# Performance work log

Measured on AMD Instinct MI355X. Metric: run time of the kernel, lower is better.

The kernel has to match this reference:

```python
import jax, jax.numpy as jnp
import numpy as np

BINS = 10
LOSS_WEIGHT = 1.0


def setup_inputs() -> dict:
    key = jax.random.key(0)
    k1, k2 = jax.random.split(key)
    N, C = 32768, 1024
    pred = jax.random.normal(k1, (N, C), dtype=jnp.float32)
    target = jax.random.randint(k2, (N,), 0, C, dtype=jnp.int32)
    return {"pred": pred, "target": target}


def reference(pred, target):
    N, C = pred.shape
    # one-hot target (torch scatter_ of 1 at label index)
    t = jax.nn.one_hot(target, C, dtype=pred.dtype)  # [N, C]
    # gradient norm g = |sigmoid(pred).detach() - target|, in [0, 1]
    g = jnp.abs(jax.nn.sigmoid(jax.lax.stop_gradient(pred)) - t)
    # all samples valid (label_weight=None -> ones); tot = max(sum(valid), 1)
    tot = jnp.asarray(N * C, dtype=pred.dtype)
    # edges = arange(bins+1)/bins with edges[-1] += 1e-6: bin = floor(g*bins),
    # g == 1.0 falls in last bin -> clip to bins-1
    bin_idx = jnp.clip((g * BINS).astype(jnp.int32), 0, BINS - 1)  # [N, C]
    counts = jnp.bincount(bin_idx.ravel(), length=BINS).astype(pred.dtype)  # [BINS]
    nonempty = counts > 0
    n = jnp.maximum(jnp.sum(nonempty).astype(pred.dtype), 1.0)
    # per-bin weight tot/num_in_bin for nonempty bins, then divide by n
    w_bin = jnp.where(nonempty, tot / jnp.maximum(counts, 1.0), 0.0) / n
    weights = w_bin[bin_idx]  # gather back to [N, C]
    # stable BCE-with-logits, weighted, reduction='sum'
    bce = jnp.maximum(pred, 0.0) - pred * t + jnp.log1p(jnp.exp(-jnp.abs(pred)))
    loss = jnp.sum(weights * bce) / tot
    return loss * LOSS_WEIGHT
```

## Files before the change

kernel.cpp:

```cpp
#include <hip/hip_runtime.h>
#include <math.h>


#define BLK 256
#define GRID 2048

typedef float v4f __attribute__((ext_vector_type(4)));

__device__ __constant__ float kT[9] = {
    -2.1972246f, -1.3862944f, -0.84729786f, -0.40546511f, 0.0f,
    0.40546511f, 0.84729786f, 1.3862944f, 2.1972246f};

__device__ __forceinline__ void wave_red(float& v) {
#pragma unroll
    for (int off = 32; off > 0; off >>= 1) v += __shfl_down(v, off, 64);
}
__device__ __forceinline__ void wave_red(int& v) {
#pragma unroll
    for (int off = 32; off > 0; off >>= 1) v += __shfl_down(v, off, 64);
}

__device__ __forceinline__ void upd(float x, float (&S)[10], int (&cnt)[9]) {
    float en = __expf(-fabsf(x));
    float bce = fmaxf(x, 0.0f) + __logf(1.0f + en);
    S[0] += bce;
#pragma unroll
    for (int q = 0; q < 9; ++q) {
        bool b = (x >= kT[q]);
        S[q + 1] += b ? bce : 0.0f;
        cnt[q] += b ? 1 : 0;
    }
}

__device__ __forceinline__ void upd_corr(float p, float (&S)[10], int (&cnt)[9]) {
    float en = __expf(-fabsf(p));
    float l1p = __logf(1.0f + en);
    float bf = fmaxf(p, 0.0f) + l1p;
    float bt = fmaxf(-p, 0.0f) + l1p;
    S[0] += bt - bf;
#pragma unroll
    for (int q = 0; q < 9; ++q) {
        bool btq = (-p >= kT[q]);
        bool bfq = (p >= kT[q]);
        S[q + 1] += (btq ? bt : 0.0f) - (bfq ? bf : 0.0f);
        cnt[q] += (btq ? 1 : 0) - (bfq ? 1 : 0);
    }
}

__global__ __launch_bounds__(BLK, 8) void ghmc_pass1(
    const float* __restrict__ pred, const int* __restrict__ target,
    float* __restrict__ blk, unsigned total4, unsigned totalNC, int N, int C) {
    float S[10];
    int cnt[9];
#pragma unroll
    for (int i = 0; i < 10; ++i) S[i] = 0.0f;
#pragma unroll
    for (int i = 0; i < 9; ++i) cnt[i] = 0;

    unsigned tid = blockIdx.x * blockDim.x + threadIdx.x;
    unsigned stride = gridDim.x * blockDim.x;
    const v4f* p4 = (const v4f*)pred;

    unsigned v = tid;
    for (; v + stride < total4; v += 2u * stride) {
        v4f a = p4[v];
        v4f b = p4[v + stride];
        upd(a[0], S, cnt);
        upd(a[1], S, cnt);
        upd(a[2], S, cnt);
        upd(a[3], S, cnt);
        upd(b[0], S, cnt);
        upd(b[1], S, cnt);
        upd(b[2], S, cnt);
        upd(b[3], S, cnt);
    }
    for (; v < total4; v += stride) {
        v4f a = p4[v];
        upd(a[0], S, cnt);
        upd(a[1], S, cnt);
        upd(a[2], S, cnt);
        upd(a[3], S, cnt);
    }

    if (tid == 0) {
        for (unsigned e = total4 << 2; e < totalNC; ++e) upd(pred[e], S, cnt);
    }

    int row = (int)tid;
    if (row < N) {
        int t = target[row];
        float p = pred[(unsigned)row * (unsigned)C + (unsigned)t];
        upd_corr(p, S, cnt);
    }

#pragma unroll
    for (int i = 0; i < 10; ++i) wave_red(S[i]);
#pragma unroll
    for (int i = 0; i < 9; ++i) wave_red(cnt[i]);

    __shared__ float sS[BLK / 64][10];
    __shared__ int sC[BLK / 64][9];
    int wid = threadIdx.x >> 6;
    int lane = threadIdx.x & 63;
    if (lane == 0) {
#pragma unroll
        for (int i = 0; i < 10; ++i) sS[wid][i] = S[i];
#pragma unroll
        for (int i = 0; i < 9; ++i) sC[wid][i] = cnt[i];
    }
    __syncthreads();
    if (threadIdx.x == 0) {
        const int nw = BLK / 64;
        float o[19];
#pragma unroll
        for (int i = 0; i < 10; ++i) {
            float a = 0.0f;
            for (int w = 0; w < nw; ++w) a += sS[w][i];
            o[i] = a;
        }
#pragma unroll
        for (int i = 0; i < 9; ++i) {
            int a = 0;
            for (int w = 0; w < nw; ++w) a += sC[w][i];
            o[10 + i] = (float)a;
        }
        float* dst = blk + (unsigned)blockIdx.x * 20u;
#pragma unroll
        for (int i = 0; i < 19; ++i) dst[i] = o[i];
    }
}

__global__ __launch_bounds__(256) void ghmc_pass2(
    const float* __restrict__ blk, float* __restrict__ out, int nblocks,
    float totalNC) {
    float P[19];
#pragma unroll
    for (int i = 0; i < 19; ++i) P[i] = 0.0f;

    for (int b = threadIdx.x; b < nblocks; b += 256) {
        const float* src = blk + (unsigned)b * 20u;
#pragma unroll
        for (int i = 0; i < 19; ++i) P[i] += src[i];
    }
#pragma unroll
    for (int i = 0; i < 19; ++i) wave_red(P[i]);

    __shared__ float sP[4][19];
    int wid = threadIdx.x >> 6;
    int lane = threadIdx.x & 63;
    if (lane == 0) {
#pragma unroll
        for (int i = 0; i < 19; ++i) sP[wid][i] = P[i];
    }
    __syncthreads();
    if (threadIdx.x == 0) {
        float Sv[11], Cv[11];
        for (int i = 0; i < 19; ++i) {
            float a = 0.0f;
            for (int w = 0; w < 4; ++w) a += sP[w][i];
            P[i] = a;
        }
        for (int i = 0; i < 10; ++i) Sv[i] = P[i];
        Sv[10] = 0.0f;
        Cv[0] = totalNC;
        for (int i = 1; i < 10; ++i) Cv[i] = P[9 + i];
        Cv[10] = 0.0f;

        int nonempty = 0;
        for (int b = 0; b < 10; ++b)
            if (Cv[b] - Cv[b + 1] > 0.5f) nonempty++;
        float n = fmaxf((float)nonempty, 1.0f);

        float loss = 0.0f;
        for (int b = 0; b < 10; ++b) {
            float c = Cv[b] - Cv[b + 1];
            if (c > 0.5f) loss += (Sv[b] - Sv[b + 1]) / (c * n);
        }
        out[0] = loss;
    }
}

extern "C" void kernel_launch(void* const* d_in, const int* in_sizes, int n_in,
                              void* d_out, int out_size, void* d_ws, size_t ws_size,
                              hipStream_t stream) {
    const float* pred = (const float*)d_in[0];
    const int* target = (const int*)d_in[1];
    int NC = in_sizes[0];
    int N = in_sizes[1];
    int C = NC / N;
    unsigned total4 = (unsigned)(NC / 4);

    int blocks = GRID;
    size_t per_block = 20 * sizeof(float);
    if (ws_size < (size_t)blocks * per_block) {
        size_t maxb = ws_size / per_block;
        blocks = (int)(maxb > 0 ? maxb : 1);
    }

    float* blkbuf = (float*)d_ws;

    ghmc_pass1<<<blocks, BLK, 0, stream>>>(pred, target, blkbuf, total4,
                                           (unsigned)NC, N, C);
    ghmc_pass2<<<1, 256, 0, stream>>>(blkbuf, (float*)d_out, blocks, (float)NC);
}
```

Measured before the change: 202.0 us.

## Replace cumulative threshold register accumulators with per-lane LDS bin histograms

Each element now gets a direct bin index from the threshold compares, and its BCE and count are added with atomics into a lane-private shared-memory histogram. This replaces the nine cumulative conditional sum and count updates per element. The target-correction path and the final per-block reduction are changed to match, and pass2 now reads direct per-bin sums. The main loop also loads four vectors per iteration instead of two. The intent is to cut VALU work per element, at the cost of two LDS atomic read-modify-writes per element and extra shared memory, which may lower occupancy.

```diff
diff --git a/kernel.cpp b/kernel.cpp
--- a/kernel.cpp
+++ b/kernel.cpp
@@ -4,6 +4,7 @@
 
 #define BLK 256
 #define GRID 2048
+#define NW (BLK / 64)
 
 typedef float v4f __attribute__((ext_vector_type(4)));
 
@@ -15,166 +16,161 @@
 #pragma unroll
     for (int off = 32; off > 0; off >>= 1) v += __shfl_down(v, off, 64);
 }
-__device__ __forceinline__ void wave_red(int& v) {
-#pragma unroll
-    for (int off = 32; off > 0; off >>= 1) v += __shfl_down(v, off, 64);
-}
-
-__device__ __forceinline__ void upd(float x, float (&S)[10], int (&cnt)[9]) {
+
+__device__ __forceinline__ void upd(float x, float* __restrict__ sumB,
+                                    float* __restrict__ cntB) {
     float en = __expf(-fabsf(x));
     float bce = fmaxf(x, 0.0f) + __logf(1.0f + en);
-    S[0] += bce;
-#pragma unroll
-    for (int q = 0; q < 9; ++q) {
-        bool b = (x >= kT[q]);
-        S[q + 1] += b ? bce : 0.0f;
-        cnt[q] += b ? 1 : 0;
-    }
-}
-
-__device__ __forceinline__ void upd_corr(float p, float (&S)[10], int (&cnt)[9]) {
+    int j = 0;
+#pragma unroll
+    for (int q = 0; q < 9; ++q) j += (x >= kT[q]) ? 1 : 0;
+    atomicAdd(sumB + (j << 6), bce);
+    atomicAdd(cntB + (j << 6), 1.0f);
+}
+
+__device__ __forceinline__ void upd_corr(float p, float* __restrict__ sumB,
+                                         float* __restrict__ cntB) {
     float en = __expf(-fabsf(p));
     float l1p = __logf(1.0f + en);
     float bf = fmaxf(p, 0.0f) + l1p;
     float bt = fmaxf(-p, 0.0f) + l1p;
-    S[0] += bt - bf;
+    int jf = 0, jt = 0;
 #pragma unroll
     for (int q = 0; q < 9; ++q) {
-        bool btq = (-p >= kT[q]);
-        bool bfq = (p >= kT[q]);
-        S[q + 1] += (btq ? bt : 0.0f) - (bfq ? bf : 0.0f);
-        cnt[q] += (btq ? 1 : 0) - (bfq ? 1 : 0);
-    }
+        jf += (p >= kT[q]) ? 1 : 0;
+        jt += (-p >= kT[q]) ? 1 : 0;
+    }
+    atomicAdd(sumB + (jf << 6), -bf);
+    atomicAdd(cntB + (jf << 6), -1.0f);
+    atomicAdd(sumB + (jt << 6), bt);
+    atomicAdd(cntB + (jt << 6), 1.0f);
 }
 
 __global__ __launch_bounds__(BLK, 8) void ghmc_pass1(
     const float* __restrict__ pred, const int* __restrict__ target,
     float* __restrict__ blk, unsigned total4, unsigned totalNC, int N, int C) {
-    float S[10];
-    int cnt[9];
-#pragma unroll
-    for (int i = 0; i < 10; ++i) S[i] = 0.0f;
-#pragma unroll
-    for (int i = 0; i < 9; ++i) cnt[i] = 0;
+    __shared__ float sSum[NW][10][64];
+    __shared__ float sCnt[NW][10][64];
+
+    int wid = threadIdx.x >> 6;
+    int lane = threadIdx.x & 63;
+    float* sumB = &sSum[wid][0][lane];
+    float* cntB = &sCnt[wid][0][lane];
+#pragma unroll
+    for (int b = 0; b < 10; ++b) {
+        sumB[b << 6] = 0.0f;
+        cntB[b << 6] = 0.0f;
+    }
 
     unsigned tid = blockIdx.x * blockDim.x + threadIdx.x;
     unsigned stride = gridDim.x * blockDim.x;
     const v4f* p4 = (const v4f*)pred;
 
     unsigned v = tid;
-    for (; v + stride < total4; v += 2u * stride) {
+    for (; v + 3u * stride < total4; v += 4u * stride) {
         v4f a = p4[v];
         v4f b = p4[v + stride];
-        upd(a[0], S, cnt);
-        upd(a[1], S, cnt);
-        upd(a[2], S, cnt);
-        upd(a[3], S, cnt);
-        upd(b[0], S, cnt);
-        upd(b[1], S, cnt);
-        upd(b[2], S, cnt);
-        upd(b[3], S, cnt);
+        v4f c = p4[v + 2u * stride];
+        v4f d = p4[v + 3u * stride];
+        upd(a[0], sumB, cntB);
+        upd(a[1], sumB, cntB);
+        upd(a[2], sumB, cntB);
+        upd(a[3], sumB, cntB);
+        upd(b[0], sumB, cntB);
+        upd(b[1], sumB, cntB);
+        upd(b[2], sumB, cntB);
+        upd(b[3], sumB, cntB);
+        upd(c[0], sumB, cntB);
+        upd(c[1], sumB, cntB);
+        upd(c[2], sumB, cntB);
+        upd(c[3], sumB, cntB);
+        upd(d[0], sumB, cntB);
+        upd(d[1], sumB, cntB);
+        upd(d[2], sumB, cntB);
+        upd(d[3], sumB, cntB);
     }
     for (; v < total4; v += stride) {
         v4f a = p4[v];
-        upd(a[0], S, cnt);
-        upd(a[1], S, cnt);
-        upd(a[2], S, cnt);
-        upd(a[3], S, cnt);
+        upd(a[0], sumB, cntB);
+        upd(a[1], sumB, cntB);
+        upd(a[2], sumB, cntB);
+        upd(a[3], sumB, cntB);
     }
 
     if (tid == 0) {
-        for (unsigned e = total4 << 2; e < totalNC; ++e) upd(pred[e], S, cnt);
+        for (unsigned e = total4 << 2; e < totalNC; ++e) upd(pred[e], sumB, cntB);
     }
 
     int row = (int)tid;
     if (row < N) {
         int t = target[row];
         float p = pred[(unsigned)row * (unsigned)C + (unsigned)t];
-        upd_corr(p, S, cnt);
-    }
-
-#pragma unroll
-    for (int i = 0; i < 10; ++i) wave_red(S[i]);
-#pragma unroll
-    for (int i = 0; i < 9; ++i) wave_red(cnt[i]);
-
-    __shared__ float sS[BLK / 64][10];
-    __shared__ int sC[BLK / 64][9];
+        upd_corr(p, sumB, cntB);
+    }
+
+    __syncthreads();
+
+    float* dst = blk + (unsigned)blockIdx.x * 20u;
+    if (wid == 0) {
+#pragma unroll
+        for (int b = 0; b < 10; ++b) {
+            float s = 0.0f;
+#pragma unroll
+            for (int w = 0; w < NW; ++w) s += sSum[w][b][lane];
+            wave_red(s);
+            if (lane == 0) dst[b] = s;
+        }
+    } else if (wid == 1) {
+#pragma unroll
+        for (int b = 0; b < 10; ++b) {
+            float c = 0.0f;
+#pragma unroll
+            for (int w = 0; w < NW; ++w) c += sCnt[w][b][lane];
+            wave_red(c);
+            if (lane == 0) dst[10 + b] = c;
+        }
+    }
+}
+
+__global__ __launch_bounds__(256) void ghmc_pass2(
+    const float* __restrict__ blk, float* __restrict__ out, int nblocks,
+    float totalNC) {
+    float P[20];
+#pragma unroll
+    for (int i = 0; i < 20; ++i) P[i] = 0.0f;
+
+    for (int b = threadIdx.x; b < nblocks; b += 256) {
+        const float* src = blk + (unsigned)b * 20u;
+#pragma unroll
+        for (int i = 0; i < 20; ++i) P[i] += src[i];
+    }
+#pragma unroll
+    for (int i = 0; i < 20; ++i) wave_red(P[i]);
+
+    __shared__ float sP[4][20];
     int wid = threadIdx.x >> 6;
     int lane = threadIdx.x & 63;
     if (lane == 0) {
 #pragma unroll
-        for (int i = 0; i < 10; ++i) sS[wid][i] = S[i];
-#pragma unroll
-        for (int i = 0; i < 9; ++i) sC[wid][i] = cnt[i];
+        for (int i = 0; i < 20; ++i) sP[wid][i] = P[i];
     }
     __syncthreads();
     if (threadIdx.x == 0) {
-        const int nw = BLK / 64;
-        float o[19];
-#pragma unroll
-        for (int i = 0; i < 10; ++i) {
-            float a = 0.0f;
-            for (int w = 0; w < nw; ++w) a += sS[w][i];
-            o[i] = a;
-        }
-#pragma unroll
-        for (int i = 0; i < 9; ++i) {
-            int a = 0;
-            for (int w = 0; w < nw; ++w) a += sC[w][i];
-            o[10 + i] = (float)a;
-        }
-        float* dst = blk + (unsigned)blockIdx.x * 20u;
-#pragma unroll
-        for (int i = 0; i < 19; ++i) dst[i] = o[i];
-    }
-}
-
-__global__ __launch_bounds__(256) void ghmc_pass2(
-    const float* __restrict__ blk, float* __restrict__ out, int nblocks,
-    float totalNC) {
-    float P[19];
-#pragma unroll
-    for (int i = 0; i < 19; ++i) P[i] = 0.0f;
-
-    for (int b = threadIdx.x; b < nblocks; b += 256) {
-        const float* src = blk + (unsigned)b * 20u;
-#pragma unroll
-        for (int i = 0; i < 19; ++i) P[i] += src[i];
-    }
-#pragma unroll
-    for (int i = 0; i < 19; ++i) wave_red(P[i]);
-
-    __shared__ float sP[4][19];
-    int wid = threadIdx.x >> 6;
-    int lane = threadIdx.x & 63;
-    if (lane == 0) {
-#pragma unroll
-        for (int i = 0; i < 19; ++i) sP[wid][i] = P[i];
-    }
-    __syncthreads();
-    if (threadIdx.x == 0) {
-        float Sv[11], Cv[11];
-        for (int i = 0; i < 19; ++i) {
+#pragma unroll
+        for (int i = 0; i < 20; ++i) {
             float a = 0.0f;
             for (int w = 0; w < 4; ++w) a += sP[w][i];
             P[i] = a;
         }
-        for (int i = 0; i < 10; ++i) Sv[i] = P[i];
-        Sv[10] = 0.0f;
-        Cv[0] = totalNC;
-        for (int i = 1; i < 10; ++i) Cv[i] = P[9 + i];
-        Cv[10] = 0.0f;
-
         int nonempty = 0;
         for (int b = 0; b < 10; ++b)
-            if (Cv[b] - Cv[b + 1] > 0.5f) nonempty++;
+            if (P[10 + b] > 0.5f) nonempty++;
         float n = fmaxf((float)nonempty, 1.0f);
 
         float loss = 0.0f;
         for (int b = 0; b < 10; ++b) {
-            float c = Cv[b] - Cv[b + 1];
-            if (c > 0.5f) loss += (Sv[b] - Sv[b + 1]) / (c * n);
+            float c = P[10 + b];
+            if (c > 0.5f) loss += P[b] / (c * n);
         }
         out[0] = loss;
     }
```

New measurement: 487.5 us. 2.41x slower.

## Pack bin count and BCE sum into one biased float accumulator with packed math

Applied to the files above, without the earlier changes.

Each threshold accumulator now adds bce+4096 instead of keeping separate float sums and int counts, and the count is later recovered with rintf(sum/4096). Two elements are processed at once in v2f accumulators so the compiler can use packed FP32 adds, and the main loop is unrolled to four vector loads per iteration. This roughly halves the per-element compare/select/add work and adds more loads in flight. The risk is precision: each thread accumulates around 64 elements per bin, so biased sums reach about 2.6e5, where float ulp is about 0.03. That rounding error accumulates into the recovered BCE sums.

```diff
diff --git a/kernel.cpp b/kernel.cpp
--- a/kernel.cpp
+++ b/kernel.cpp
@@ -4,8 +4,11 @@
 
 #define BLK 256
 #define GRID 2048
+#define BIAS 4096.0f
+#define INV_BIAS (1.0f / 4096.0f)
 
 typedef float v4f __attribute__((ext_vector_type(4)));
+typedef float v2f __attribute__((ext_vector_type(2)));
 
 __device__ __constant__ float kT[9] = {
     -2.1972246f, -1.3862944f, -0.84729786f, -0.40546511f, 0.0f,
@@ -15,82 +18,99 @@
 #pragma unroll
     for (int off = 32; off > 0; off >>= 1) v += __shfl_down(v, off, 64);
 }
-__device__ __forceinline__ void wave_red(int& v) {
-#pragma unroll
-    for (int off = 32; off > 0; off >>= 1) v += __shfl_down(v, off, 64);
-}
-
-__device__ __forceinline__ void upd(float x, float (&S)[10], int (&cnt)[9]) {
+
+__device__ __forceinline__ void upd2(float xa, float xb, v2f& S0, v2f (&A)[9]) {
+    float ena = __expf(-fabsf(xa));
+    float enb = __expf(-fabsf(xb));
+    float la = __logf(1.0f + ena);
+    float lb = __logf(1.0f + enb);
+    v2f bc;
+    bc.x = fmaxf(xa, 0.0f) + la;
+    bc.y = fmaxf(xb, 0.0f) + lb;
+    S0 += bc;
+    v2f bb = bc + (v2f)(BIAS);
+#pragma unroll
+    for (int q = 0; q < 9; ++q) {
+        v2f t;
+        t.x = (xa >= kT[q]) ? bb.x : 0.0f;
+        t.y = (xb >= kT[q]) ? bb.y : 0.0f;
+        A[q] += t;
+    }
+}
+
+__device__ __forceinline__ void upd1(float x, v2f& S0, v2f (&A)[9]) {
     float en = __expf(-fabsf(x));
     float bce = fmaxf(x, 0.0f) + __logf(1.0f + en);
-    S[0] += bce;
-#pragma unroll
-    for (int q = 0; q < 9; ++q) {
-        bool b = (x >= kT[q]);
-        S[q + 1] += b ? bce : 0.0f;
-        cnt[q] += b ? 1 : 0;
-    }
-}
-
-__device__ __forceinline__ void upd_corr(float p, float (&S)[10], int (&cnt)[9]) {
-    float en = __expf(-fabsf(p));
-    float l1p = __logf(1.0f + en);
-    float bf = fmaxf(p, 0.0f) + l1p;
-    float bt = fmaxf(-p, 0.0f) + l1p;
-    S[0] += bt - bf;
-#pragma unroll
-    for (int q = 0; q < 9; ++q) {
-        bool btq = (-p >= kT[q]);
-        bool bfq = (p >= kT[q]);
-        S[q + 1] += (btq ? bt : 0.0f) - (bfq ? bf : 0.0f);
-        cnt[q] += (btq ? 1 : 0) - (bfq ? 1 : 0);
-    }
+    S0.x += bce;
+    float bb = bce + BIAS;
+#pragma unroll
+    for (int q = 0; q < 9; ++q) A[q].x += (x >= kT[q]) ? bb : 0.0f;
 }
 
 __global__ __launch_bounds__(BLK, 8) void ghmc_pass1(
     const float* __restrict__ pred, const int* __restrict__ target,
     float* __restrict__ blk, unsigned total4, unsigned totalNC, int N, int C) {
-    float S[10];
-    int cnt[9];
-#pragma unroll
-    for (int i = 0; i < 10; ++i) S[i] = 0.0f;
-#pragma unroll
-    for (int i = 0; i < 9; ++i) cnt[i] = 0;
+    v2f S0 = (v2f)(0.0f);
+    v2f A[9];
+#pragma unroll
+    for (int q = 0; q < 9; ++q) A[q] = (v2f)(0.0f);
 
     unsigned tid = blockIdx.x * blockDim.x + threadIdx.x;
     unsigned stride = gridDim.x * blockDim.x;
     const v4f* p4 = (const v4f*)pred;
 
     unsigned v = tid;
-    for (; v + stride < total4; v += 2u * stride) {
+    for (; v + 3u * stride < total4; v += 4u * stride) {
         v4f a = p4[v];
         v4f b = p4[v + stride];
-        upd(a[0], S, cnt);
-        upd(a[1], S, cnt);
-        upd(a[2], S, cnt);
-        upd(a[3], S, cnt);
-        upd(b[0], S, cnt);
-        upd(b[1], S, cnt);
-        upd(b[2], S, cnt);
-        upd(b[3], S, cnt);
+        v4f c = p4[v + 2u * stride];
+        v4f d = p4[v + 3u * stride];
+        upd2(a[0], a[1], S0, A);
+        upd2(a[2], a[3], S0, A);
+        upd2(b[0], b[1], S0, A);
+        upd2(b[2], b[3], S0, A);
+        upd2(c[0], c[1], S0, A);
+        upd2(c[2], c[3], S0, A);
+        upd2(d[0], d[1], S0, A);
+        upd2(d[2], d[3], S0, A);
     }
     for (; v < total4; v += stride) {
         v4f a = p4[v];
-        upd(a[0], S, cnt);
-        upd(a[1], S, cnt);
-        upd(a[2], S, cnt);
-        upd(a[3], S, cnt);
+        upd2(a[0], a[1], S0, A);
+        upd2(a[2], a[3], S0, A);
     }
 
     if (tid == 0) {
-        for (unsigned e = total4 << 2; e < totalNC; ++e) upd(pred[e], S, cnt);
+        for (unsigned e = total4 << 2; e < totalNC; ++e) upd1(pred[e], S0, A);
+    }
+
+    float S[10];
+    float cnt[9];
+    S[0] = S0.x + S0.y;
+#pragma unroll
+    for (int q = 0; q < 9; ++q) {
+        float sp = A[q].x + A[q].y;
+        float c = rintf(sp * INV_BIAS);
+        cnt[q] = c;
+        S[q + 1] = fmaf(c, -BIAS, sp);
     }
 
     int row = (int)tid;
     if (row < N) {
         int t = target[row];
         float p = pred[(unsigned)row * (unsigned)C + (unsigned)t];
-        upd_corr(p, S, cnt);
+        float en = __expf(-fabsf(p));
+        float l1p = __logf(1.0f + en);
+        float bf = fmaxf(p, 0.0f) + l1p;
+        float bt = fmaxf(-p, 0.0f) + l1p;
+        S[0] += bt - bf;
+#pragma unroll
+        for (int q = 0; q < 9; ++q) {
+            bool btq = (-p >= kT[q]);
+            bool bfq = (p >= kT[q]);
+            S[q + 1] += (btq ? bt : 0.0f) - (bfq ? bf : 0.0f);
+            cnt[q] += (btq ? 1.0f : 0.0f) - (bfq ? 1.0f : 0.0f);
+        }
     }
 
 #pragma unroll
@@ -99,7 +119,7 @@
     for (int i = 0; i < 9; ++i) wave_red(cnt[i]);
 
     __shared__ float sS[BLK / 64][10];
-    __shared__ int sC[BLK / 64][9];
+    __shared__ float sC[BLK / 64][9];
     int wid = threadIdx.x >> 6;
     int lane = threadIdx.x & 63;
     if (lane == 0) {
@@ -120,9 +140,9 @@
         }
 #pragma unroll
         for (int i = 0; i < 9; ++i) {
-            int a = 0;
+            float a = 0.0f;
             for (int w = 0; w < nw; ++w) a += sC[w][i];
-            o[10 + i] = (float)a;
+            o[10 + i] = a;
         }
         float* dst = blk + (unsigned)blockIdx.x * 20u;
 #pragma unroll
```

New measurement: 204.1 us. Within noise of the previous version (+1.0%).
